# Performance work log

Hardware: AMD Instinct MI355X
Metric: run time of the kernel (lower is better)

The kernel has to match this reference:

```python
import jax, jax.numpy as jnp
import numpy as np

NUM_CLASSES = 81
THRESHOLD = 0.5
NEGPOS_RATIO = 3
ALPHA = 1.0
VAR0, VAR1 = 0.1, 0.2  # cfg['variance']
B, P, NOBJ = 64, 8732, 16


def setup_inputs() -> dict:
    key = jax.random.key(0)
    k1, k2, k3, k4, k5, k6, k7 = jax.random.split(key, 7)
    loc_data = jax.random.normal(k1, (B, P, 4), jnp.float32)
    conf_data = jax.random.normal(k2, (B, P, NUM_CLASSES), jnp.float32)
    # priors in center form (cx, cy, w, h), all in (0,1)
    centers = jax.random.uniform(k3, (P, 2), minval=0.05, maxval=0.95)
    sizes = jax.random.uniform(k4, (P, 2), minval=0.05, maxval=0.5)
    priors = jnp.concatenate([centers, sizes], axis=1).astype(jnp.float32)
    # targets: [B, NOBJ, 5] = (x1, y1, x2, y2, label), valid boxes with x1<x2
    tl = jax.random.uniform(k5, (B, NOBJ, 2), maxval=0.6)
    wh = jax.random.uniform(k6, (B, NOBJ, 2), minval=0.05, maxval=0.35)
    labels = jax.random.randint(k7, (B, NOBJ, 1), 0, NUM_CLASSES - 1).astype(jnp.float32)
    targets = jnp.concatenate([tl, tl + wh, labels], axis=2)
    return {"loc_data": loc_data, "conf_data": conf_data, "priors": priors, "targets": targets}


def point_form(boxes):
    # (cx,cy,w,h) -> (x1,y1,x2,y2)
    return jnp.concatenate([boxes[:, :2] - boxes[:, 2:] / 2,
                            boxes[:, :2] + boxes[:, 2:] / 2], axis=1)


def jaccard(a, b):
    # a: [n,4], b: [m,4], point form -> IoU [n,m]
    tl = jnp.maximum(a[:, None, :2], b[None, :, :2])
    br = jnp.minimum(a[:, None, 2:], b[None, :, 2:])
    wh = jnp.clip(br - tl, 0.0)
    inter = wh[..., 0] * wh[..., 1]
    area_a = ((a[:, 2] - a[:, 0]) * (a[:, 3] - a[:, 1]))[:, None]
    area_b = ((b[:, 2] - b[:, 0]) * (b[:, 3] - b[:, 1]))[None, :]
    return inter / (area_a + area_b - inter)


def encode(matched, priors):
    # matched: [P,4] point form GT, priors: [P,4] center form
    g_cxcy = (matched[:, :2] + matched[:, 2:]) / 2 - priors[:, :2]
    g_cxcy = g_cxcy / (VAR0 * priors[:, 2:])
    g_wh = jnp.log((matched[:, 2:] - matched[:, :2]) / priors[:, 2:]) / VAR1
    return jnp.concatenate([g_cxcy, g_wh], axis=1)


def match_one(truths, labels, priors):
    # truths: [NOBJ,4] point form, labels: [NOBJ]
    overlaps = jaccard(truths, point_form(priors))  # [NOBJ, P]
    best_prior_idx = jnp.argmax(overlaps, axis=1)   # [NOBJ]
    best_truth_overlap = jnp.max(overlaps, axis=0)  # [P]
    best_truth_idx = jnp.argmax(overlaps, axis=0)   # [P]
    # ensure every GT keeps its best prior
    best_truth_overlap = best_truth_overlap.at[best_prior_idx].set(2.0)
    best_truth_idx = best_truth_idx.at[best_prior_idx].set(jnp.arange(truths.shape[0]))
    matched = truths[best_truth_idx]                        # [P,4]
    conf = (labels[best_truth_idx] + 1).astype(jnp.int32)   # [P]
    conf = jnp.where(best_truth_overlap < THRESHOLD, 0, conf)
    return encode(matched, priors), conf


def smooth_l1(x):
    ax = jnp.abs(x)
    return jnp.where(ax < 1.0, 0.5 * x * x, ax - 0.5)


def reference(loc_data, conf_data, priors, targets):
    truths = targets[..., :4]
    labels = targets[..., 4]
    loc_t, conf_t = jax.vmap(match_one, in_axes=(0, 0, None))(truths, labels, priors)
    loc_t = jax.lax.stop_gradient(loc_t)  # targets are non-grad in the original
    pos = conf_t > 0                       # [B,P]
    num_pos = pos.sum(axis=1)              # [B]
    # localization loss (smooth L1, sum over positives)
    loss_l = jnp.sum(smooth_l1(loc_data - loc_t) * pos[..., None].astype(loc_data.dtype))
    # per-prior CE = logsumexp(logits) - logit[target]
    lse = jax.nn.logsumexp(conf_data, axis=2)                                   # [B,P]
    gathered = jnp.take_along_axis(conf_data, conf_t[..., None], axis=2)[..., 0]
    loss_c = lse - gathered                                                      # [B,P]
    # hard negative mining: rank negatives by loss, keep top 3*num_pos
    loss_c_mine = jnp.where(pos, 0.0, loss_c)
    idx_rank = jnp.argsort(jnp.argsort(-loss_c_mine, axis=1), axis=1)
    num_neg = jnp.minimum(NEGPOS_RATIO * num_pos, P - 1)
    neg = idx_rank < num_neg[:, None]
    sel = jnp.logical_or(pos, neg)
    loss_conf = jnp.sum(jnp.where(sel, loss_c, 0.0))
    N = num_pos.sum().astype(loc_data.dtype)
    return ALPHA * loss_l / N + loss_conf / N
```

## Files before the change

### kernel.cpp

```cpp
#include <hip/hip_runtime.h>

#define BB 64
#define PP 8732
#define NOBJ 16
#define NC 81
#define THRESH 0.5f
#define NEGPOS 3
#define NCHUNK 4
#define CHUNK (PP / NCHUNK)

#define TK_THREADS 512
#define TK_KEYS 18

__device__ __forceinline__ float smooth_l1(float x) {
    float ax = fabsf(x);
    return (ax < 1.0f) ? 0.5f * x * x : ax - 0.5f;
}

__global__ __launch_bounds__(256) void k_matchA(
    const float* __restrict__ priors, const float* __restrict__ targets,
    unsigned long long* __restrict__ g_best)
{
    const int chunk = blockIdx.x;
    const int b = blockIdx.y;
    const int tid = threadIdx.x;

    __shared__ float s_tx1[NOBJ], s_ty1[NOBJ], s_tx2[NOBJ], s_ty2[NOBJ];
    __shared__ float s_area[NOBJ];
    __shared__ unsigned long long s_best[NOBJ];

    if (tid < NOBJ) {
        const float* t = targets + ((size_t)b * NOBJ + tid) * 5;
        float x1 = t[0], y1 = t[1], x2 = t[2], y2 = t[3];
        s_tx1[tid] = x1; s_ty1[tid] = y1; s_tx2[tid] = x2; s_ty2[tid] = y2;
        s_area[tid] = (x2 - x1) * (y2 - y1);
        s_best[tid] = 0ull;
    }
    __syncthreads();

    unsigned long long best[NOBJ];
    #pragma unroll
    for (int t = 0; t < NOBJ; ++t) best[t] = 0ull;

    const int p0 = chunk * CHUNK, p1 = p0 + CHUNK;
    for (int p = p0 + tid; p < p1; p += 256) {
        float4 pr = ((const float4*)priors)[p];
        float px1 = pr.x - pr.z * 0.5f, py1 = pr.y - pr.w * 0.5f;
        float px2 = pr.x + pr.z * 0.5f, py2 = pr.y + pr.w * 0.5f;
        float pa = (px2 - px1) * (py2 - py1);
        unsigned revp = 0xFFFFFFFFu - (unsigned)p;
        #pragma unroll
        for (int t = 0; t < NOBJ; ++t) {
            float ix1 = fmaxf(s_tx1[t], px1), iy1 = fmaxf(s_ty1[t], py1);
            float ix2 = fminf(s_tx2[t], px2), iy2 = fminf(s_ty2[t], py2);
            float iw = fmaxf(ix2 - ix1, 0.f), ih = fmaxf(iy2 - iy1, 0.f);
            float inter = iw * ih;
            float iou = inter / (s_area[t] + pa - inter);
            unsigned long long key =
                ((unsigned long long)__float_as_uint(iou) << 32) | revp;
            if (key > best[t]) best[t] = key;
        }
    }
    #pragma unroll
    for (int t = 0; t < NOBJ; ++t) {
        unsigned long long v = best[t];
        for (int o = 32; o > 0; o >>= 1) {
            unsigned long long w = __shfl_down(v, o);
            if (w > v) v = w;
        }
        if ((tid & 63) == 0) atomicMax(&s_best[t], v);
    }
    __syncthreads();
    if (tid < NOBJ) atomicMax(&g_best[b * NOBJ + tid], s_best[tid]);
}

__global__ __launch_bounds__(256) void k_matchB(
    const float* __restrict__ loc_data, const float* __restrict__ priors,
    const float* __restrict__ targets, const unsigned long long* __restrict__ g_best,
    unsigned char* __restrict__ conf_t, int* __restrict__ num_pos,
    double* __restrict__ accum)
{
    const int chunk = blockIdx.x;
    const int b = blockIdx.y;
    const int tid = threadIdx.x;

    __shared__ float s_tx1[NOBJ], s_ty1[NOBJ], s_tx2[NOBJ], s_ty2[NOBJ];
    __shared__ float s_lab[NOBJ], s_area[NOBJ];
    __shared__ int s_bpi[NOBJ];

    if (tid < NOBJ) {
        const float* t = targets + ((size_t)b * NOBJ + tid) * 5;
        float x1 = t[0], y1 = t[1], x2 = t[2], y2 = t[3];
        s_tx1[tid] = x1; s_ty1[tid] = y1; s_tx2[tid] = x2; s_ty2[tid] = y2;
        s_lab[tid] = t[4];
        s_area[tid] = (x2 - x1) * (y2 - y1);
        unsigned revp = (unsigned)(g_best[b * NOBJ + tid] & 0xFFFFFFFFull);
        s_bpi[tid] = (int)(0xFFFFFFFFu - revp);
    }
    __syncthreads();

    int n_pos = 0;
    float lloss = 0.f;
    const int p0 = chunk * CHUNK, p1 = p0 + CHUNK;
    for (int p = p0 + tid; p < p1; p += 256) {
        float4 pr = ((const float4*)priors)[p];
        float px1 = pr.x - pr.z * 0.5f, py1 = pr.y - pr.w * 0.5f;
        float px2 = pr.x + pr.z * 0.5f, py2 = pr.y + pr.w * 0.5f;
        float pa = (px2 - px1) * (py2 - py1);
        float bt_ov = -1.f;
        int bt_idx = 0;
        #pragma unroll
        for (int t = 0; t < NOBJ; ++t) {
            float ix1 = fmaxf(s_tx1[t], px1), iy1 = fmaxf(s_ty1[t], py1);
            float ix2 = fminf(s_tx2[t], px2), iy2 = fminf(s_ty2[t], py2);
            float iw = fmaxf(ix2 - ix1, 0.f), ih = fmaxf(iy2 - iy1, 0.f);
            float inter = iw * ih;
            float iou = inter / (s_area[t] + pa - inter);
            if (iou > bt_ov) { bt_ov = iou; bt_idx = t; }
        }
        #pragma unroll
        for (int i = 0; i < NOBJ; ++i)
            if (s_bpi[i] == p) { bt_idx = i; bt_ov = 2.0f; }

        int c = (bt_ov < THRESH) ? 0 : ((int)s_lab[bt_idx] + 1);
        conf_t[(size_t)b * PP + p] = (unsigned char)c;

        if (c > 0) {
            n_pos++;
            float mx1 = s_tx1[bt_idx], my1 = s_ty1[bt_idx];
            float mx2 = s_tx2[bt_idx], my2 = s_ty2[bt_idx];
            float gcx = ((mx1 + mx2) * 0.5f - pr.x) / (0.1f * pr.z);
            float gcy = ((my1 + my2) * 0.5f - pr.y) / (0.1f * pr.w);
            float gw = logf((mx2 - mx1) / pr.z) / 0.2f;
            float gh = logf((my2 - my1) / pr.w) / 0.2f;
            float4 ld = ((const float4*)loc_data)[(size_t)b * PP + p];
            lloss += smooth_l1(ld.x - gcx) + smooth_l1(ld.y - gcy) +
                     smooth_l1(ld.z - gw) + smooth_l1(ld.w - gh);
        }
    }

    for (int o = 32; o > 0; o >>= 1) {
        n_pos += __shfl_down(n_pos, o);
        lloss += __shfl_down(lloss, o);
    }
    __shared__ int s_np[4];
    __shared__ float s_ll[4];
    int wave = tid >> 6, lane = tid & 63;
    if (lane == 0) { s_np[wave] = n_pos; s_ll[wave] = lloss; }
    __syncthreads();
    if (tid == 0) {
        atomicAdd(&num_pos[b], s_np[0] + s_np[1] + s_np[2] + s_np[3]);
        atomicAdd(&accum[0], (double)(s_ll[0] + s_ll[1] + s_ll[2] + s_ll[3]));
    }
}

__global__ __launch_bounds__(256) void k_conf(
    const float* __restrict__ conf_data, const unsigned char* __restrict__ conf_t,
    float* __restrict__ lcm, double* __restrict__ accum)
{
    __shared__ float4 s_buf4[2][648];
    const int tid = threadIdx.x;
    const int r = tid >> 3;
    const int s = tid & 7;
    const int seg_start = s * 10;
    const int seg_len = (s == 7) ? 11 : 10;
    const int base_row = blockIdx.x * 256;
    const float4* g4base = (const float4*)conf_data;

    float4 t0, t1, t2;
    {
        const float4* g4 = g4base + (size_t)base_row * NC / 4;
        t0 = g4[tid]; t1 = g4[tid + 256];
        if (tid < 136) t2 = g4[tid + 512];
    }

    float posl = 0.f;
    for (int h = 0; h < 8; ++h) {
        float4* buf = s_buf4[h & 1];
        buf[tid] = t0; buf[tid + 256] = t1;
        if (tid < 136) buf[tid + 512] = t2;
        if (h + 1 < 8) {
            const float4* g4 = g4base + (size_t)(base_row + (h + 1) * 32) * NC / 4;
            t0 = g4[tid]; t1 = g4[tid + 256];
            if (tid < 136) t2 = g4[tid + 512];
        }
        __syncthreads();

        const float* myrow = (const float*)buf + r * NC;
        float v[11];
        #pragma unroll
        for (int j = 0; j < 11; ++j) v[j] = myrow[seg_start + j];

        float m = -1e30f;
        #pragma unroll
        for (int j = 0; j < 11; ++j) m = fmaxf(m, (j < seg_len) ? v[j] : -1e30f);
        m = fmaxf(m, __shfl_xor(m, 1));
        m = fmaxf(m, __shfl_xor(m, 2));
        m = fmaxf(m, __shfl_xor(m, 4));
        float e = 0.f;
        #pragma unroll
        for (int j = 0; j < 11; ++j) e += (j < seg_len) ? __expf(v[j] - m) : 0.f;
        e += __shfl_xor(e, 1);
        e += __shfl_xor(e, 2);
        e += __shfl_xor(e, 4);

        if (s == 0) {
            int row = base_row + h * 32 + r;
            int c = (int)conf_t[row];
            float lse = m + __logf(e);
            float lc = lse - myrow[c];
            bool pos = c > 0;
            lcm[row] = pos ? 0.f : lc;
            if (pos) posl += lc;
        }
    }
    for (int o = 32; o > 0; o >>= 1) posl += __shfl_down(posl, o);
    __shared__ float s_w[4];
    if ((tid & 63) == 0) s_w[tid >> 6] = posl;
    __syncthreads();
    if (tid == 0)
        atomicAdd(&accum[1], (double)(s_w[0] + s_w[1] + s_w[2] + s_w[3]));
}

__global__ __launch_bounds__(TK_THREADS) void k_topk(
    const float* __restrict__ lcm, const int* __restrict__ num_pos,
    double* __restrict__ accum, int* __restrict__ done_cnt,
    float* __restrict__ out)
{
    const int b = blockIdx.x, tid = threadIdx.x;
    unsigned key[TK_KEYS];
    #pragma unroll
    for (int j = 0; j < TK_KEYS; ++j) {
        int i = tid + j * TK_THREADS;
        key[j] = (i < PP) ? __float_as_uint(lcm[(size_t)b * PP + i]) : 0u;
    }
    __shared__ int s_cnt[32];
    if (tid < 32) s_cnt[tid] = 0;
    int k = NEGPOS * num_pos[b];
    if (k > PP - 1) k = PP - 1;
    __syncthreads();

    unsigned T = 0;
    for (int bit = 30; bit >= 0; --bit) {
        unsigned cand = T | (1u << bit);
        int cnt = 0;
        #pragma unroll
        for (int j = 0; j < TK_KEYS; ++j)
            cnt += (int)__popcll(__ballot(key[j] >= cand));
        if ((tid & 63) == 0) atomicAdd(&s_cnt[bit], cnt);
        __syncthreads();
        if (s_cnt[bit] >= k) T = cand;
    }

    float sum = 0.f;
    int cgt = 0;
    #pragma unroll
    for (int j = 0; j < TK_KEYS; ++j) {
        if (key[j] > T) { sum += __uint_as_float(key[j]); cgt++; }
    }
    for (int o = 32; o > 0; o >>= 1) {
        sum += __shfl_down(sum, o);
        cgt += __shfl_down(cgt, o);
    }
    __shared__ float s_s[8];
    __shared__ int s_c[8];
    if ((tid & 63) == 0) { s_s[tid >> 6] = sum; s_c[tid >> 6] = cgt; }
    __syncthreads();
    if (tid == 0) {
        float tot = 0.f; int ctot = 0;
        for (int w = 0; w < 8; ++w) { tot += s_s[w]; ctot += s_c[w]; }
        float neg = tot + (float)(k - ctot) * __uint_as_float(T);
        atomicAdd(&accum[1], (double)neg);
        __threadfence();
        int prev = atomicAdd(done_cnt, 1);
        if (prev == BB - 1) {
            double a0 = atomicAdd(&accum[0], 0.0);
            double a1 = atomicAdd(&accum[1], 0.0);
            int N = 0;
            for (int bb = 0; bb < BB; ++bb) N += num_pos[bb];
            out[0] = (float)((a0 + a1) / (double)N);
        }
    }
}

extern "C" void kernel_launch(void* const* d_in, const int* in_sizes, int n_in,
                              void* d_out, int out_size, void* d_ws, size_t ws_size,
                              hipStream_t stream) {
    const float* loc_data  = (const float*)d_in[0];
    const float* conf_data = (const float*)d_in[1];
    const float* priors    = (const float*)d_in[2];
    const float* targets   = (const float*)d_in[3];

    char* ws = (char*)d_ws;
    double* accum = (double*)ws;
    int* done_cnt = (int*)(ws + 16);
    int* num_pos = (int*)(ws + 32);
    unsigned long long* g_best = (unsigned long long*)(ws + 512);
    unsigned char* conf_t = (unsigned char*)(ws + 8704);
    float* lcm = (float*)(ws + 8704 + (size_t)BB * PP);

    hipMemsetAsync(ws, 0, 8704, stream);

    dim3 mg(NCHUNK, BB);
    k_matchA<<<mg, 256, 0, stream>>>(priors, targets, g_best);
    k_matchB<<<mg, 256, 0, stream>>>(loc_data, priors, targets, g_best,
                                     conf_t, num_pos, accum);

    k_conf<<<(BB * PP) / 256, 256, 0, stream>>>(conf_data, conf_t, lcm, accum);

    k_topk<<<BB, TK_THREADS, 0, stream>>>(lcm, num_pos, accum, done_cnt,
                                          (float*)d_out);
}
```

Measured before the change: 327.8 us.

## Fuse matching kernels, drop memset, use radix-histogram top-k selection

Merges the two matching kernels into a single per-batch 1024-thread kernel that finds best priors in shared memory, then computes conf_t and the localization loss. This removes the global g_best atomics, one launch and the memset, with accumulators reset inside the kernel. The top-k threshold search switches from 31 bitwise ballot rounds to 4 rounds of 8-bit radix histograms. The trade-off is less parallelism in matching (64 blocks instead of 256) and shared-memory atomic contention in the histogram.

```diff
diff --git a/kernel.cpp b/kernel.cpp
--- a/kernel.cpp
+++ b/kernel.cpp
@@ -6,8 +6,6 @@
 #define NC 81
 #define THRESH 0.5f
 #define NEGPOS 3
-#define NCHUNK 4
-#define CHUNK (PP / NCHUNK)
 
 #define TK_THREADS 512
 #define TK_KEYS 18
@@ -17,33 +15,40 @@
     return (ax < 1.0f) ? 0.5f * x * x : ax - 0.5f;
 }
 
-__global__ __launch_bounds__(256) void k_matchA(
-    const float* __restrict__ priors, const float* __restrict__ targets,
-    unsigned long long* __restrict__ g_best)
+__global__ __launch_bounds__(1024) void k_match(
+    const float* __restrict__ loc_data, const float* __restrict__ priors,
+    const float* __restrict__ targets,
+    unsigned char* __restrict__ conf_t, int* __restrict__ num_pos,
+    float* __restrict__ lloss_b, double* __restrict__ accum,
+    int* __restrict__ done_cnt)
 {
-    const int chunk = blockIdx.x;
-    const int b = blockIdx.y;
+    const int b = blockIdx.x;
     const int tid = threadIdx.x;
 
     __shared__ float s_tx1[NOBJ], s_ty1[NOBJ], s_tx2[NOBJ], s_ty2[NOBJ];
-    __shared__ float s_area[NOBJ];
+    __shared__ float s_lab[NOBJ], s_area[NOBJ];
     __shared__ unsigned long long s_best[NOBJ];
+    __shared__ int s_bpi[NOBJ];
 
     if (tid < NOBJ) {
         const float* t = targets + ((size_t)b * NOBJ + tid) * 5;
         float x1 = t[0], y1 = t[1], x2 = t[2], y2 = t[3];
         s_tx1[tid] = x1; s_ty1[tid] = y1; s_tx2[tid] = x2; s_ty2[tid] = y2;
+        s_lab[tid] = t[4];
         s_area[tid] = (x2 - x1) * (y2 - y1);
         s_best[tid] = 0ull;
     }
+    if (b == 0 && tid == 0) {
+        accum[0] = 0.0; accum[1] = 0.0;
+        done_cnt[0] = 0;
+    }
     __syncthreads();
 
     unsigned long long best[NOBJ];
     #pragma unroll
     for (int t = 0; t < NOBJ; ++t) best[t] = 0ull;
 
-    const int p0 = chunk * CHUNK, p1 = p0 + CHUNK;
-    for (int p = p0 + tid; p < p1; p += 256) {
+    for (int p = tid; p < PP; p += 1024) {
         float4 pr = ((const float4*)priors)[p];
         float px1 = pr.x - pr.z * 0.5f, py1 = pr.y - pr.w * 0.5f;
         float px2 = pr.x + pr.z * 0.5f, py2 = pr.y + pr.w * 0.5f;
@@ -71,38 +76,13 @@
         if ((tid & 63) == 0) atomicMax(&s_best[t], v);
     }
     __syncthreads();
-    if (tid < NOBJ) atomicMax(&g_best[b * NOBJ + tid], s_best[tid]);
-}
-
-__global__ __launch_bounds__(256) void k_matchB(
-    const float* __restrict__ loc_data, const float* __restrict__ priors,
-    const float* __restrict__ targets, const unsigned long long* __restrict__ g_best,
-    unsigned char* __restrict__ conf_t, int* __restrict__ num_pos,
-    double* __restrict__ accum)
-{
-    const int chunk = blockIdx.x;
-    const int b = blockIdx.y;
-    const int tid = threadIdx.x;
-
-    __shared__ float s_tx1[NOBJ], s_ty1[NOBJ], s_tx2[NOBJ], s_ty2[NOBJ];
-    __shared__ float s_lab[NOBJ], s_area[NOBJ];
-    __shared__ int s_bpi[NOBJ];
-
-    if (tid < NOBJ) {
-        const float* t = targets + ((size_t)b * NOBJ + tid) * 5;
-        float x1 = t[0], y1 = t[1], x2 = t[2], y2 = t[3];
-        s_tx1[tid] = x1; s_ty1[tid] = y1; s_tx2[tid] = x2; s_ty2[tid] = y2;
-        s_lab[tid] = t[4];
-        s_area[tid] = (x2 - x1) * (y2 - y1);
-        unsigned revp = (unsigned)(g_best[b * NOBJ + tid] & 0xFFFFFFFFull);
-        s_bpi[tid] = (int)(0xFFFFFFFFu - revp);
-    }
+    if (tid < NOBJ)
+        s_bpi[tid] = (int)(0xFFFFFFFFu - (unsigned)(s_best[tid] & 0xFFFFFFFFull));
     __syncthreads();
 
     int n_pos = 0;
     float lloss = 0.f;
-    const int p0 = chunk * CHUNK, p1 = p0 + CHUNK;
-    for (int p = p0 + tid; p < p1; p += 256) {
+    for (int p = tid; p < PP; p += 1024) {
         float4 pr = ((const float4*)priors)[p];
         float px1 = pr.x - pr.z * 0.5f, py1 = pr.y - pr.w * 0.5f;
         float px2 = pr.x + pr.z * 0.5f, py2 = pr.y + pr.w * 0.5f;
@@ -143,14 +123,16 @@
         n_pos += __shfl_down(n_pos, o);
         lloss += __shfl_down(lloss, o);
     }
-    __shared__ int s_np[4];
-    __shared__ float s_ll[4];
-    int wave = tid >> 6, lane = tid & 63;
-    if (lane == 0) { s_np[wave] = n_pos; s_ll[wave] = lloss; }
+    __shared__ int s_np[16];
+    __shared__ float s_ll[16];
+    if ((tid & 63) == 0) { s_np[tid >> 6] = n_pos; s_ll[tid >> 6] = lloss; }
     __syncthreads();
     if (tid == 0) {
-        atomicAdd(&num_pos[b], s_np[0] + s_np[1] + s_np[2] + s_np[3]);
-        atomicAdd(&accum[0], (double)(s_ll[0] + s_ll[1] + s_ll[2] + s_ll[3]));
+        int np = 0; float ll = 0.f;
+        #pragma unroll
+        for (int w = 0; w < 16; ++w) { np += s_np[w]; ll += s_ll[w]; }
+        num_pos[b] = np;
+        lloss_b[b] = ll;
     }
 }
 
@@ -224,6 +206,7 @@
 
 __global__ __launch_bounds__(TK_THREADS) void k_topk(
     const float* __restrict__ lcm, const int* __restrict__ num_pos,
+    const float* __restrict__ lloss_b,
     double* __restrict__ accum, int* __restrict__ done_cnt,
     float* __restrict__ out)
 {
@@ -234,24 +217,56 @@
         int i = tid + j * TK_THREADS;
         key[j] = (i < PP) ? __float_as_uint(lcm[(size_t)b * PP + i]) : 0u;
     }
-    __shared__ int s_cnt[32];
-    if (tid < 32) s_cnt[tid] = 0;
+    __shared__ int s_hist[256];
+    __shared__ int s_vk[2];
     int k = NEGPOS * num_pos[b];
     if (k > PP - 1) k = PP - 1;
-    __syncthreads();
-
-    unsigned T = 0;
-    for (int bit = 30; bit >= 0; --bit) {
-        unsigned cand = T | (1u << bit);
-        int cnt = 0;
-        #pragma unroll
-        for (int j = 0; j < TK_KEYS; ++j)
-            cnt += (int)__popcll(__ballot(key[j] >= cand));
-        if ((tid & 63) == 0) atomicAdd(&s_cnt[bit], cnt);
+
+    unsigned P = 0;
+    int kk = k;
+    #pragma unroll
+    for (int rd = 0; rd < 4; ++rd) {
+        const int shift = 24 - 8 * rd;
+        if (tid < 256) s_hist[tid] = 0;
         __syncthreads();
-        if (s_cnt[bit] >= k) T = cand;
-    }
-
+        const unsigned hi_mask = (rd == 0) ? 0u : (0xFFFFFFFFu << (shift + 8));
+        #pragma unroll
+        for (int j = 0; j < TK_KEYS; ++j) {
+            int i = tid + j * TK_THREADS;
+            if (i < PP && (((key[j] ^ P) & hi_mask) == 0u))
+                atomicAdd(&s_hist[(key[j] >> shift) & 255], 1);
+        }
+        __syncthreads();
+        if (tid < 64) {
+            int h0 = s_hist[4 * tid + 0], h1 = s_hist[4 * tid + 1];
+            int h2 = s_hist[4 * tid + 2], h3 = s_hist[4 * tid + 3];
+            int s3 = h3, s2 = h2 + s3, s1 = h1 + s2, s0 = h0 + s1;
+            int acc = s0;
+            #pragma unroll
+            for (int o = 1; o < 64; o <<= 1) {
+                int t = __shfl_down(acc, o);
+                if (tid + o < 64) acc += t;
+            }
+            int excl = acc - s0;
+            int c0 = s0 + excl, c1 = s1 + excl, c2 = s2 + excl, c3 = s3 + excl;
+            unsigned long long m = __ballot(c0 >= kk);
+            int L = 63 - __clzll(m);
+            if (tid == L) {
+                int vi, cnext;
+                if (c3 >= kk)      { vi = 3; cnext = excl; }
+                else if (c2 >= kk) { vi = 2; cnext = c3; }
+                else if (c1 >= kk) { vi = 1; cnext = c2; }
+                else               { vi = 0; cnext = c1; }
+                s_vk[0] = 4 * tid + vi;
+                s_vk[1] = kk - cnext;
+            }
+        }
+        __syncthreads();
+        P |= ((unsigned)s_vk[0]) << shift;
+        kk = s_vk[1];
+    }
+
+    const unsigned T = P;
     float sum = 0.f;
     int cgt = 0;
     #pragma unroll
@@ -274,11 +289,13 @@
         __threadfence();
         int prev = atomicAdd(done_cnt, 1);
         if (prev == BB - 1) {
-            double a0 = atomicAdd(&accum[0], 0.0);
             double a1 = atomicAdd(&accum[1], 0.0);
-            int N = 0;
-            for (int bb = 0; bb < BB; ++bb) N += num_pos[bb];
-            out[0] = (float)((a0 + a1) / (double)N);
+            int N = 0; double ll = 0.0;
+            for (int bb = 0; bb < BB; ++bb) {
+                N += num_pos[bb];
+                ll += (double)lloss_b[bb];
+            }
+            out[0] = (float)((ll + a1) / (double)N);
         }
     }
 }
@@ -295,19 +312,16 @@
     double* accum = (double*)ws;
     int* done_cnt = (int*)(ws + 16);
     int* num_pos = (int*)(ws + 32);
-    unsigned long long* g_best = (unsigned long long*)(ws + 512);
+    float* lloss_b = (float*)(ws + 288);
     unsigned char* conf_t = (unsigned char*)(ws + 8704);
     float* lcm = (float*)(ws + 8704 + (size_t)BB * PP);
 
-    hipMemsetAsync(ws, 0, 8704, stream);
-
-    dim3 mg(NCHUNK, BB);
-    k_matchA<<<mg, 256, 0, stream>>>(priors, targets, g_best);
-    k_matchB<<<mg, 256, 0, stream>>>(loc_data, priors, targets, g_best,
-                                     conf_t, num_pos, accum);
+
+    k_match<<<BB, 1024, 0, stream>>>(loc_data, priors, targets,
+                                     conf_t, num_pos, lloss_b, accum, done_cnt);
 
     k_conf<<<(BB * PP) / 256, 256, 0, stream>>>(conf_data, conf_t, lcm, accum);
 
-    k_topk<<<BB, TK_THREADS, 0, stream>>>(lcm, num_pos, accum, done_cnt,
+    k_topk<<<BB, TK_THREADS, 0, stream>>>(lcm, num_pos, lloss_b, accum, done_cnt,
                                           (float*)d_out);
 }
```

Measured after the change: 433.5 us. +32.3%, slower.
